# Kernel optimization log

Measured on AMD Instinct MI355X. Metric: run time of the kernel, lower is better.

## Reference

```python
import jax, jax.numpy as jnp
import numpy as np

B, N, F_IN, F_HID, F_OUT = 64, 1024, 64, 128, 64

def setup_inputs() -> dict:
    key = jax.random.key(0)
    ks = jax.random.split(key, 6)
    x = jax.random.normal(ks[0], (B, N, F_IN), dtype=jnp.float32)
    adj = jax.random.uniform(ks[1], (B, N, N), dtype=jnp.float32)
    mask = jax.random.randint(ks[2], (B, N), 0, 2).astype(bool)
    W1 = jax.random.normal(ks[3], (F_IN, F_HID), dtype=jnp.float32) * (1.0 / np.sqrt(F_IN))
    b1 = jnp.zeros((F_HID,), dtype=jnp.float32)
    W2 = jax.random.normal(ks[4], (F_HID, F_OUT), dtype=jnp.float32) * (1.0 / np.sqrt(F_HID))
    b2 = jnp.zeros((F_OUT,), dtype=jnp.float32)
    eps = jnp.zeros((1,), dtype=jnp.float32)
    return {"x": x, "adj": adj, "mask": mask, "W1": W1, "b1": b1, "W2": W2, "b2": b2, "eps": eps}

def reference(x, adj, mask, W1, b1, W2, b2, eps):
    # neighbor aggregation: out[b,i,f] = sum_j adj[b,i,j] * x[b,j,f]
    agg = jnp.einsum('bij,bjf->bif', adj, x)
    # add_loop=True: (1 + eps) * x + aggregated neighbors
    h = (1.0 + eps[0]) * x + agg
    # 2-layer GIN MLP applied per node (only valid nodes contribute in the
    # torch version via gather/scatter; invalid positions are zeroed)
    h = jax.nn.relu(h @ W1 + b1) @ W2 + b2
    return jnp.where(mask[..., None], h, jnp.zeros((), dtype=h.dtype))
```

## Files before the change

kernel.cpp:

```cpp
#include <hip/hip_runtime.h>


#define N_     1024
#define FIN    64
#define FHID   128
#define FOUT   64
#define HS_LD  68
#define H1_LD  132
#define CH     64
#define NCHUNK 16
#define KSPC   4
#define FROW   9
#define AUNITS 18
#define BUFU   1152

typedef __attribute__((ext_vector_type(16))) float f32x16;
typedef __attribute__((ext_vector_type(8)))  short s16x8;
typedef __attribute__((ext_vector_type(4)))  short s16x4;

__device__ inline short f2bf(float f) {
    union { float f; unsigned int u; } v; v.f = f;
    unsigned int r = v.u + 0x7fffu + ((v.u >> 16) & 1u);
    return (short)(r >> 16);
}

__global__ __launch_bounds__(256) void xt_pack(const float* __restrict__ x,
                                               s16x8* __restrict__ xt)
{
    const int g  = blockIdx.x * 256 + threadIdx.x;
    const int n  = g & 31;
    const int ng = (g >> 5) & 1;
    const int ks = (g >> 6) & 63;
    const int b  = g >> 12;
    const int f  = ng * 32 + n;

    s16x8 u0, u1;
    #pragma unroll
    for (int k = 0; k < 8; ++k)
        u0[k] = f2bf(x[(size_t)(b * N_ + ks * 16 + k) * FIN + f]);
    #pragma unroll
    for (int k = 0; k < 8; ++k)
        u1[k] = f2bf(x[(size_t)(b * N_ + ks * 16 + 8 + k) * FIN + f]);
    xt[2 * g]     = u0;
    xt[2 * g + 1] = u1;
}

__global__ __launch_bounds__(256, 3) void gin_main(
    const float* __restrict__ x, const float* __restrict__ adj,
    const int* __restrict__ mask, const float* __restrict__ W1,
    const float* __restrict__ b1, const float* __restrict__ W2,
    const float* __restrict__ b2, const float* __restrict__ epsp,
    const s16x8* __restrict__ xt, float* __restrict__ out)
{
    __shared__ __align__(16) char region_raw[33792];
    __shared__ float hs[64 * HS_LD];

    auto   asf  = reinterpret_cast<s16x8 (*)[64][FROW]>(region_raw);
    s16x4* asf4 = reinterpret_cast<s16x4*>(region_raw);
    float* h1s  = reinterpret_cast<float*>(region_raw);

    const int t    = threadIdx.x;
    const int lane = t & 63;
    const int w    = t >> 6;
    const int b    = blockIdx.x >> 4;
    const int i0   = (blockIdx.x & 15) * 64;

    const float* xb   = x   + (size_t)b * N_ * FIN;
    const float* adjb = adj + (size_t)b * N_ * N_ + (size_t)i0 * N_;

    const int l31  = lane & 31;
    const int half = lane >> 5;
    const int mrow = (w & 1) * 32;
    const int ncol = (w >> 1) * 32;
    const int ngq  = (w >> 1);

    const int rq16 = t >> 4;
    const int cl16 = t & 15;
    const float* adjA = adjb + (size_t)rq16 * N_ + cl16 * 4;

    const int bfl = l31 * 2 + half;
    const size_t bgbase = (size_t)(b * 64) * 2 + ngq;

    f32x16 acc;
    #pragma unroll
    for (int r = 0; r < 16; ++r) acc[r] = 0.f;

    float4 areg[2][4];
    s16x8  xreg[2][4];

    #pragma unroll
    for (int q = 0; q < 4; ++q)
        areg[0][q] = *reinterpret_cast<const float4*>(adjA + (size_t)q * 16 * N_);
    #pragma unroll
    for (int q = 0; q < 4; ++q)
        areg[1][q] = *reinterpret_cast<const float4*>(adjA + (size_t)q * 16 * N_ + CH);
    #pragma unroll
    for (int s = 0; s < KSPC; ++s)
        xreg[0][s] = xt[(bgbase + (size_t)s * 2) * 64 + bfl];
    #pragma unroll
    for (int s = 0; s < KSPC; ++s)
        xreg[1][s] = xt[(bgbase + (size_t)(KSPC + s) * 2) * 64 + bfl];

    #pragma unroll
    for (int q = 0; q < 4; ++q) {
        s16x4 fr;
        fr[0] = f2bf(areg[0][q].x); fr[1] = f2bf(areg[0][q].y);
        fr[2] = f2bf(areg[0][q].z); fr[3] = f2bf(areg[0][q].w);
        asf4[(q * 16 + rq16) * AUNITS + cl16] = fr;
    }
    asm volatile("s_waitcnt lgkmcnt(0)" ::: "memory");
    __builtin_amdgcn_s_barrier();

    #pragma unroll
    for (int c = 0; c < NCHUNK; ++c) {
        if (c + 2 < NCHUNK) {
            #pragma unroll
            for (int q = 0; q < 4; ++q)
                areg[c & 1][q] = *reinterpret_cast<const float4*>(
                    adjA + (size_t)q * 16 * N_ + (size_t)(c + 2) * CH);
        }
        #pragma unroll
        for (int s = 0; s < KSPC; ++s) {
            const s16x8 a = asf[c & 1][mrow + l31][2 * s + half];
            acc = __builtin_amdgcn_mfma_f32_32x32x16_bf16(a, xreg[c & 1][s], acc, 0, 0, 0);
        }
        if (c + 2 < NCHUNK) {
            #pragma unroll
            for (int s = 0; s < KSPC; ++s)
                xreg[c & 1][s] = xt[(bgbase + (size_t)((c + 2) * KSPC + s) * 2) * 64 + bfl];
        }
        if (c + 1 < NCHUNK) {
            const int boff = ((c + 1) & 1) * BUFU;
            #pragma unroll
            for (int q = 0; q < 4; ++q) {
                const float4 u = areg[(c + 1) & 1][q];
                s16x4 fr;
                fr[0] = f2bf(u.x); fr[1] = f2bf(u.y);
                fr[2] = f2bf(u.z); fr[3] = f2bf(u.w);
                asf4[boff + (q * 16 + rq16) * AUNITS + cl16] = fr;
            }
            asm volatile("s_waitcnt lgkmcnt(0)" ::: "memory");
            __builtin_amdgcn_s_barrier();
        }
    }

    {
        const float se = 1.0f + epsp[0];
        const int col = ncol + l31;
        #pragma unroll
        for (int reg = 0; reg < 16; ++reg) {
            const int row = mrow + (reg & 3) + 8 * (reg >> 2) + 4 * half;
            const float xv = xb[(size_t)(i0 + row) * FIN + col];
            hs[row * HS_LD + col] = acc[reg] + se * xv;
        }
    }
    __syncthreads();

    {
        const int k4 = (t & 31) * 4;
        const int rb = (t >> 5) * 8;
        float4 hacc[8];
        const float4 b1v = *reinterpret_cast<const float4*>(b1 + k4);
        #pragma unroll
        for (int r = 0; r < 8; ++r) hacc[r] = b1v;

        #pragma unroll 4
        for (int j = 0; j < FIN; ++j) {
            const float4 w1v = *reinterpret_cast<const float4*>(W1 + j * FHID + k4);
            #pragma unroll
            for (int r = 0; r < 8; ++r) {
                const float hv = hs[(rb + r) * HS_LD + j];
                hacc[r].x += hv * w1v.x; hacc[r].y += hv * w1v.y;
                hacc[r].z += hv * w1v.z; hacc[r].w += hv * w1v.w;
            }
        }
        #pragma unroll
        for (int r = 0; r < 8; ++r) {
            float4 v;
            v.x = fmaxf(hacc[r].x, 0.f); v.y = fmaxf(hacc[r].y, 0.f);
            v.z = fmaxf(hacc[r].z, 0.f); v.w = fmaxf(hacc[r].w, 0.f);
            *reinterpret_cast<float4*>(&h1s[(rb + r) * H1_LD + k4]) = v;
        }
    }
    __syncthreads();

    {
        const int fi = (t & 15) * 4;
        const int ri = (t >> 4) * 4;
        float4 oacc[4];
        const float4 b2v = *reinterpret_cast<const float4*>(b2 + fi);
        #pragma unroll
        for (int ii = 0; ii < 4; ++ii) oacc[ii] = b2v;

        #pragma unroll 4
        for (int j = 0; j < FHID; ++j) {
            const float4 w2v = *reinterpret_cast<const float4*>(W2 + j * FOUT + fi);
            #pragma unroll
            for (int ii = 0; ii < 4; ++ii) {
                const float hv = h1s[(ri + ii) * H1_LD + j];
                oacc[ii].x += hv * w2v.x; oacc[ii].y += hv * w2v.y;
                oacc[ii].z += hv * w2v.z; oacc[ii].w += hv * w2v.w;
            }
        }
        #pragma unroll
        for (int ii = 0; ii < 4; ++ii) {
            const int gi = i0 + ri + ii;
            const int m  = mask[b * N_ + gi];
            float4 o = oacc[ii];
            if (!m) o = make_float4(0.f, 0.f, 0.f, 0.f);
            *reinterpret_cast<float4*>(out + ((size_t)b * N_ + gi) * FOUT + fi) = o;
        }
    }
}

extern "C" void kernel_launch(void* const* d_in, const int* in_sizes, int n_in,
                              void* d_out, int out_size, void* d_ws, size_t ws_size,
                              hipStream_t stream) {
    const float* x    = (const float*)d_in[0];
    const float* adj  = (const float*)d_in[1];
    const int*   mask = (const int*)  d_in[2];
    const float* W1   = (const float*)d_in[3];
    const float* b1   = (const float*)d_in[4];
    const float* W2   = (const float*)d_in[5];
    const float* b2   = (const float*)d_in[6];
    const float* eps  = (const float*)d_in[7];
    float* out = (float*)d_out;
    s16x8* xt = (s16x8*)d_ws;

    xt_pack<<<dim3(1024), dim3(256), 0, stream>>>(x, xt);
    gin_main<<<dim3(64 * 16), dim3(256), 0, stream>>>(x, adj, mask, W1, b1, W2, b2, eps, xt, out);
}
```

Before: 422.9 us.

## Fuse x bf16 packing into main kernel via LDS staging

Removes the separate xt_pack pre-pass kernel and instead has each block load fp32 x rows for the current K chunk, convert them to bf16 and stage them in a double-buffered LDS region alongside the adjacency tile. MFMA B operands are now read from LDS rather than from a global pre-packed buffer. This saves a kernel launch and the global round trip of the packed copy. In exchange every one of the 16 row-blocks per batch converts the same x again, and LDS use and register pressure per block rise slightly.

```diff
diff --git a/kernel.cpp b/kernel.cpp
--- a/kernel.cpp
+++ b/kernel.cpp
@@ -12,7 +12,9 @@
 #define KSPC   4
 #define FROW   9
 #define AUNITS 18
-#define BUFU   1152
+#define ABUFU  1152
+#define ADJ_BYTES 18432
+#define XSU    512
 
 typedef __attribute__((ext_vector_type(16))) float f32x16;
 typedef __attribute__((ext_vector_type(8)))  short s16x8;
@@ -24,39 +26,19 @@
     return (short)(r >> 16);
 }
 
-__global__ __launch_bounds__(256) void xt_pack(const float* __restrict__ x,
-                                               s16x8* __restrict__ xt)
-{
-    const int g  = blockIdx.x * 256 + threadIdx.x;
-    const int n  = g & 31;
-    const int ng = (g >> 5) & 1;
-    const int ks = (g >> 6) & 63;
-    const int b  = g >> 12;
-    const int f  = ng * 32 + n;
-
-    s16x8 u0, u1;
-    #pragma unroll
-    for (int k = 0; k < 8; ++k)
-        u0[k] = f2bf(x[(size_t)(b * N_ + ks * 16 + k) * FIN + f]);
-    #pragma unroll
-    for (int k = 0; k < 8; ++k)
-        u1[k] = f2bf(x[(size_t)(b * N_ + ks * 16 + 8 + k) * FIN + f]);
-    xt[2 * g]     = u0;
-    xt[2 * g + 1] = u1;
-}
-
 __global__ __launch_bounds__(256, 3) void gin_main(
     const float* __restrict__ x, const float* __restrict__ adj,
     const int* __restrict__ mask, const float* __restrict__ W1,
     const float* __restrict__ b1, const float* __restrict__ W2,
     const float* __restrict__ b2, const float* __restrict__ epsp,
-    const s16x8* __restrict__ xt, float* __restrict__ out)
+    float* __restrict__ out)
 {
-    __shared__ __align__(16) char region_raw[33792];
+    __shared__ __align__(16) char region_raw[34816];
     __shared__ float hs[64 * HS_LD];
 
     auto   asf  = reinterpret_cast<s16x8 (*)[64][FROW]>(region_raw);
     s16x4* asf4 = reinterpret_cast<s16x4*>(region_raw);
+    s16x8* xsb  = reinterpret_cast<s16x8*>(region_raw + ADJ_BYTES);
     float* h1s  = reinterpret_cast<float*>(region_raw);
 
     const int t    = threadIdx.x;
@@ -78,67 +60,55 @@
     const int cl16 = t & 15;
     const float* adjA = adjb + (size_t)rq16 * N_ + cl16 * 4;
 
-    const int bfl = l31 * 2 + half;
-    const size_t bgbase = (size_t)(b * 64) * 2 + ngq;
+    const int gx = t >> 5;
+    const int mx = t & 31;
+    const float* xrow0 = xb + (size_t)(gx * 8) * FIN + 2 * mx;
+    const int slotA = gx * 64 + mx;
+
+    const int sbase = ngq * 16 + (l31 >> 1) + ((l31 & 1) << 5);
 
     f32x16 acc;
     #pragma unroll
     for (int r = 0; r < 16; ++r) acc[r] = 0.f;
 
     float4 areg[2][4];
-    s16x8  xreg[2][4];
-
-    #pragma unroll
-    for (int q = 0; q < 4; ++q)
-        areg[0][q] = *reinterpret_cast<const float4*>(adjA + (size_t)q * 16 * N_);
-    #pragma unroll
-    for (int q = 0; q < 4; ++q)
-        areg[1][q] = *reinterpret_cast<const float4*>(adjA + (size_t)q * 16 * N_ + CH);
-    #pragma unroll
-    for (int s = 0; s < KSPC; ++s)
-        xreg[0][s] = xt[(bgbase + (size_t)s * 2) * 64 + bfl];
-    #pragma unroll
-    for (int s = 0; s < KSPC; ++s)
-        xreg[1][s] = xt[(bgbase + (size_t)(KSPC + s) * 2) * 64 + bfl];
-
-    #pragma unroll
-    for (int q = 0; q < 4; ++q) {
-        s16x4 fr;
-        fr[0] = f2bf(areg[0][q].x); fr[1] = f2bf(areg[0][q].y);
-        fr[2] = f2bf(areg[0][q].z); fr[3] = f2bf(areg[0][q].w);
-        asf4[(q * 16 + rq16) * AUNITS + cl16] = fr;
-    }
+    float2 xregf[2][8];
+
+    #define ISSUE_A(p, c_) { _Pragma("unroll") for (int q = 0; q < 4; ++q) \
+        areg[p][q] = *reinterpret_cast<const float4*>(adjA + (size_t)q * 16 * N_ + (size_t)(c_) * CH); }
+    #define ISSUE_X(p, c_) { _Pragma("unroll") for (int k = 0; k < 8; ++k) \
+        xregf[p][k] = *reinterpret_cast<const float2*>(xrow0 + (size_t)((c_) * CH + k) * FIN); }
+    #define STAGE_A(o, p) { _Pragma("unroll") for (int q = 0; q < 4; ++q) { \
+        const float4 u = areg[p][q]; s16x4 fr; \
+        fr[0] = f2bf(u.x); fr[1] = f2bf(u.y); fr[2] = f2bf(u.z); fr[3] = f2bf(u.w); \
+        asf4[(o) * ABUFU + (q * 16 + rq16) * AUNITS + cl16] = fr; } }
+    #define STAGE_X(o, p) { s16x8 frA, frB; \
+        _Pragma("unroll") for (int k = 0; k < 8; ++k) { \
+            frA[k] = f2bf(xregf[p][k].x); frB[k] = f2bf(xregf[p][k].y); } \
+        xsb[(o) * XSU + slotA] = frA; xsb[(o) * XSU + slotA + 32] = frB; }
+
+    ISSUE_A(0, 0); ISSUE_A(1, 1);
+    ISSUE_X(0, 0); ISSUE_X(1, 1);
+    STAGE_A(0, 0);
+    STAGE_X(0, 0);
     asm volatile("s_waitcnt lgkmcnt(0)" ::: "memory");
     __builtin_amdgcn_s_barrier();
 
     #pragma unroll
     for (int c = 0; c < NCHUNK; ++c) {
         if (c + 2 < NCHUNK) {
-            #pragma unroll
-            for (int q = 0; q < 4; ++q)
-                areg[c & 1][q] = *reinterpret_cast<const float4*>(
-                    adjA + (size_t)q * 16 * N_ + (size_t)(c + 2) * CH);
+            ISSUE_A(c & 1, c + 2);
+            ISSUE_X(c & 1, c + 2);
         }
         #pragma unroll
         for (int s = 0; s < KSPC; ++s) {
-            const s16x8 a = asf[c & 1][mrow + l31][2 * s + half];
-            acc = __builtin_amdgcn_mfma_f32_32x32x16_bf16(a, xreg[c & 1][s], acc, 0, 0, 0);
-        }
-        if (c + 2 < NCHUNK) {
-            #pragma unroll
-            for (int s = 0; s < KSPC; ++s)
-                xreg[c & 1][s] = xt[(bgbase + (size_t)((c + 2) * KSPC + s) * 2) * 64 + bfl];
+            const s16x8 a  = asf[c & 1][mrow + l31][2 * s + half];
+            const s16x8 bb = xsb[(c & 1) * XSU + (s * 2 + half) * 64 + sbase];
+            acc = __builtin_amdgcn_mfma_f32_32x32x16_bf16(a, bb, acc, 0, 0, 0);
         }
         if (c + 1 < NCHUNK) {
-            const int boff = ((c + 1) & 1) * BUFU;
-            #pragma unroll
-            for (int q = 0; q < 4; ++q) {
-                const float4 u = areg[(c + 1) & 1][q];
-                s16x4 fr;
-                fr[0] = f2bf(u.x); fr[1] = f2bf(u.y);
-                fr[2] = f2bf(u.z); fr[3] = f2bf(u.w);
-                asf4[boff + (q * 16 + rq16) * AUNITS + cl16] = fr;
-            }
+            STAGE_A((c + 1) & 1, (c + 1) & 1);
+            STAGE_X((c + 1) & 1, (c + 1) & 1);
             asm volatile("s_waitcnt lgkmcnt(0)" ::: "memory");
             __builtin_amdgcn_s_barrier();
         }
@@ -225,8 +195,7 @@
     const float* b2   = (const float*)d_in[6];
     const float* eps  = (const float*)d_in[7];
     float* out = (float*)d_out;
-    s16x8* xt = (s16x8*)d_ws;
-
-    xt_pack<<<dim3(1024), dim3(256), 0, stream>>>(x, xt);
-    gin_main<<<dim3(64 * 16), dim3(256), 0, stream>>>(x, adj, mask, W1, b1, W2, b2, eps, xt, out);
+    (void)d_ws; (void)ws_size;
+
+    gin_main<<<dim3(64 * 16), dim3(256), 0, stream>>>(x, adj, mask, W1, b1, W2, b2, eps, out);
 }
```

New measurement: 424.0 us. Within noise of the previous version (+0.3%).
